# Kernel optimization log

Measured on AMD Instinct MI355X. Metric: run time of the kernel, lower is better.

## Reference

```python
import jax, jax.numpy as jnp
import numpy as np

B = 262144
NUM_CLASSES = 100
D = 128            # embedding_latent_dim and MLP width
VQ_DIM = 64        # vq_embedding_dim
VQ_K = 512         # vq_num_embeddings
A = 64             # action_dim
SQUISH = 1.0
COMMIT = 0.25


def _dense_params(key, fan_in, fan_out, scale=None):
    # he_uniform-like init; exact init distribution irrelevant for correctness baseline
    kw, kb = jax.random.split(key)
    lim = np.sqrt(6.0 / fan_in)
    W = jax.random.uniform(kw, (fan_in, fan_out), minval=-lim, maxval=lim, dtype=jnp.float32)
    b = jnp.zeros((fan_out,), dtype=jnp.float32)
    return W, b


def setup_inputs() -> dict:
    key = jax.random.key(0)
    ks = jax.random.split(key, 16)
    obs = jax.random.randint(ks[0], (B,), 0, NUM_CLASSES)
    embed = jax.random.normal(ks[1], (NUM_CLASSES, D), dtype=jnp.float32)
    W0, b0 = _dense_params(ks[2], D, D)
    W1, b1 = _dense_params(ks[3], D, D)
    W2, b2 = _dense_params(ks[4], D, D)
    Wp, bp = _dense_params(ks[5], D, VQ_DIM)
    lim = np.sqrt(3.0 / VQ_DIM)  # variance_scaling fan_in uniform
    vq_emb = jax.random.uniform(ks[6], (VQ_K, VQ_DIM), minval=-lim, maxval=lim, dtype=jnp.float32)
    Wa = 0.01 * jax.random.normal(ks[7], (VQ_DIM, A), dtype=jnp.float32)
    ba = jnp.zeros((A,), dtype=jnp.float32)
    Ws = 0.01 * jax.random.normal(ks[8], (VQ_DIM, A), dtype=jnp.float32)
    bs = jnp.zeros((A,), dtype=jnp.float32)
    Wc0, bc0 = _dense_params(ks[9], VQ_DIM, 128)
    Wc1, bc1 = _dense_params(ks[10], 128, 128)
    Wc2, bc2 = _dense_params(ks[11], 128, 32)
    Wc3, bc3 = _dense_params(ks[12], 32, 1)
    return dict(obs=obs, embed=embed, W0=W0, b0=b0, W1=W1, b1=b1, W2=W2, b2=b2,
                Wp=Wp, bp=bp, vq_emb=vq_emb, Wa=Wa, ba=ba, Ws=Ws, bs=bs,
                Wc0=Wc0, bc0=bc0, Wc1=Wc1, bc1=bc1, Wc2=Wc2, bc2=bc2, Wc3=Wc3, bc3=bc3)


def reference(obs, embed, W0, b0, W1, b1, W2, b2, Wp, bp, vq_emb,
              Wa, ba, Ws, bs, Wc0, bc0, Wc1, bc1, Wc2, bc2, Wc3, bc3):
    # class embedding lookup: [B, D]
    y = embed[obs]
    z = jax.nn.relu(y @ W0 + b0)
    z = jax.nn.relu(z @ W1 + b1)
    z = jax.nn.relu(z @ W2 + b2)
    z = z @ Wp + bp  # project to vq_embedding_dim: [B, 64]
    # --- VectorQuantizer ---
    # pairwise squared distances [B, K] via expansion trick
    dists = (jnp.sum(z * z, axis=1, keepdims=True)
             - 2.0 * (z @ vq_emb.T)
             + jnp.sum(vq_emb * vq_emb, axis=1)[None, :])
    encoding_indices = jnp.argmin(dists, axis=1)  # [B]
    quantized = vq_emb[encoding_indices]          # gather == onehot @ emb
    q_ste = z + jax.lax.stop_gradient(quantized - z)  # straight-through
    e_latent = jnp.mean((jax.lax.stop_gradient(q_ste) - z) ** 2)
    q_latent = jnp.mean((q_ste - jax.lax.stop_gradient(z)) ** 2)
    vq_loss = q_latent + COMMIT * e_latent
    # actor heads
    actor_mean = jax.nn.sigmoid(q_ste @ Wa + ba)
    scale_diag = jax.nn.sigmoid(q_ste @ Ws + bs) * SQUISH + 1e-8
    # critic stack
    c = jax.nn.sigmoid(q_ste @ Wc0 + bc0)
    c = jax.nn.sigmoid(c @ Wc1 + bc1)
    c = jax.nn.sigmoid(c @ Wc2 + bc2)
    critic = jnp.squeeze(c @ Wc3 + bc3, axis=-1)
    return actor_mean, scale_diag, critic, vq_loss, encoding_indices
```

## Files before the change

kernel.cpp:

```cpp
#include <hip/hip_runtime.h>
#include <hip/hip_bf16.h>
#include <math.h>

#define NCLS 100
#define DD   128
#define VQD  64
#define VQK  512

__device__ __forceinline__ float sigmoidf_(float x) { return 1.0f / (1.0f + expf(-x)); }

__global__ __launch_bounds__(128) void class_forward(
    const float* __restrict__ embed,
    const float* __restrict__ W0, const float* __restrict__ b0,
    const float* __restrict__ W1, const float* __restrict__ b1,
    const float* __restrict__ W2, const float* __restrict__ b2,
    const float* __restrict__ Wp, const float* __restrict__ bp,
    const float* __restrict__ vq,
    const float* __restrict__ Wa, const float* __restrict__ ba,
    const float* __restrict__ Ws, const float* __restrict__ bs,
    const float* __restrict__ Wc0, const float* __restrict__ bc0,
    const float* __restrict__ Wc1, const float* __restrict__ bc1,
    const float* __restrict__ Wc2, const float* __restrict__ bc2,
    const float* __restrict__ Wc3, const float* __restrict__ bc3,
    float* __restrict__ am_c, float* __restrict__ sd_c,
    float* __restrict__ cr_c, float* __restrict__ ms_c, int* __restrict__ id_c,
    unsigned int* __restrict__ counts)
{
    __shared__ float ya[128], za[128], q64[64], qs[64], red[128];
    __shared__ int   redi[128];
    const int c = blockIdx.x;
    const int t = threadIdx.x;

    if (c == 0 && t < NCLS) counts[t] = 0u;

    ya[t] = embed[c * DD + t];
    __syncthreads();

    float acc = b0[t];
    #pragma unroll 16
    for (int k = 0; k < 128; ++k) acc = fmaf(ya[k], W0[k * 128 + t], acc);
    za[t] = fmaxf(acc, 0.0f);
    __syncthreads();

    acc = b1[t];
    #pragma unroll 16
    for (int k = 0; k < 128; ++k) acc = fmaf(za[k], W1[k * 128 + t], acc);
    ya[t] = fmaxf(acc, 0.0f);
    __syncthreads();

    acc = b2[t];
    #pragma unroll 16
    for (int k = 0; k < 128; ++k) acc = fmaf(ya[k], W2[k * 128 + t], acc);
    za[t] = fmaxf(acc, 0.0f);
    __syncthreads();

    if (t < 64) {
        float a2 = bp[t];
        #pragma unroll 16
        for (int k = 0; k < 128; ++k) a2 = fmaf(za[k], Wp[k * 64 + t], a2);
        q64[t] = a2;
    }
    __syncthreads();

    if (t < 64) { red[t] = q64[t] * q64[t]; } else red[t] = 0.0f;
    __syncthreads();
    for (int s = 64; s > 0; s >>= 1) { if (t < s) red[t] += red[t + s]; __syncthreads(); }
    const float zz = red[0];
    __syncthreads();

    float bestv = 3.4e38f;
    int   besti = 0;
    for (int cc = t; cc < VQK; cc += 128) {
        const float* e = vq + cc * VQD;
        float dot = 0.0f, esq = 0.0f;
        #pragma unroll 16
        for (int k = 0; k < VQD; ++k) {
            float ev = e[k];
            dot = fmaf(q64[k], ev, dot);
            esq = fmaf(ev, ev, esq);
        }
        float d = (zz - 2.0f * dot) + esq;
        if (d < bestv) { bestv = d; besti = cc; }
    }
    red[t] = bestv; redi[t] = besti;
    __syncthreads();
    for (int s = 64; s > 0; s >>= 1) {
        if (t < s) {
            float v = red[t + s]; int i2 = redi[t + s];
            if (v < red[t] || (v == red[t] && i2 < redi[t])) { red[t] = v; redi[t] = i2; }
        }
        __syncthreads();
    }
    const int best = redi[0];
    __syncthreads();

    if (t < 64) {
        float z  = q64[t];
        float qq = vq[best * VQD + t];
        float q_ste = z + (qq - z);
        qs[t] = q_ste;
        float dd = q_ste - z;
        red[t] = dd * dd;
    } else red[t] = 0.0f;
    __syncthreads();
    for (int s = 64; s > 0; s >>= 1) { if (t < s) red[t] += red[t + s]; __syncthreads(); }
    if (t == 0) { ms_c[c] = red[0]; id_c[c] = best; }

    {
        const int j = t & 63;
        const float* W = (t < 64) ? Wa : Ws;
        float a2 = (t < 64) ? ba[j] : bs[j];
        #pragma unroll 16
        for (int k = 0; k < 64; ++k) a2 = fmaf(qs[k], W[k * 64 + j], a2);
        float s = sigmoidf_(a2);
        if (t < 64) am_c[c * 64 + j] = s;
        else        sd_c[c * 64 + j] = s * 1.0f + 1e-8f;
    }

    acc = bc0[t];
    #pragma unroll 16
    for (int k = 0; k < 64; ++k) acc = fmaf(qs[k], Wc0[k * 128 + t], acc);
    ya[t] = sigmoidf_(acc);
    __syncthreads();

    acc = bc1[t];
    #pragma unroll 16
    for (int k = 0; k < 128; ++k) acc = fmaf(ya[k], Wc1[k * 128 + t], acc);
    za[t] = sigmoidf_(acc);
    __syncthreads();

    if (t < 32) {
        float a2 = bc2[t];
        #pragma unroll 16
        for (int k = 0; k < 128; ++k) a2 = fmaf(za[k], Wc2[k * 32 + t], a2);
        q64[t] = sigmoidf_(a2);
    }
    __syncthreads();

    if (t == 0) {
        float a2 = bc3[0];
        for (int k = 0; k < 32; ++k) a2 = fmaf(q64[k], Wc3[k], a2);
        cr_c[c] = a2;
    }
}

__global__ __launch_bounds__(256) void scatter_vec(
    const int* __restrict__ obs,
    const float4* __restrict__ amc, const float4* __restrict__ sdc,
    const float* __restrict__ crc,  const int* __restrict__ idc,
    float4* __restrict__ out_am, float4* __restrict__ out_sd,
    float* __restrict__ out_cr,  float* __restrict__ out_idx, int n4)
{
    const int e4 = blockIdx.x * 256 + threadIdx.x;
    if (e4 >= n4) return;
    const int i  = e4 >> 4;
    const int d4 = e4 & 15;
    const int c  = obs[i];
    const int off = (c << 4) + d4;
    out_am[e4] = amc[off];
    out_sd[e4] = sdc[off];
    if (d4 == 0) {
        out_cr[i]  = crc[c];
        out_idx[i] = (float)idc[c];
    }
}

__global__ __launch_bounds__(256) void hist_obs(
    const int* __restrict__ obs, unsigned int* __restrict__ counts, int n)
{
    __shared__ unsigned int h[NCLS];
    const int t = threadIdx.x;
    if (t < NCLS) h[t] = 0u;
    __syncthreads();
    for (int i = blockIdx.x * blockDim.x + t; i < n; i += gridDim.x * blockDim.x)
        atomicAdd(&h[obs[i]], 1u);
    __syncthreads();
    if (t < NCLS) atomicAdd(&counts[t], h[t]);
}

__global__ __launch_bounds__(128) void finalize_vq(
    const unsigned int* __restrict__ counts, const float* __restrict__ ms,
    float* __restrict__ out, int n)
{
    __shared__ double sd[128];
    const int t = threadIdx.x;
    double a = 0.0;
    if (t < NCLS) a = (double)counts[t] * (double)ms[t];
    sd[t] = a;
    __syncthreads();
    for (int s = 64; s > 0; s >>= 1) { if (t < s) sd[t] += sd[t + s]; __syncthreads(); }
    if (t == 0) out[0] = (float)(1.25 * sd[0] / ((double)n * 64.0));
}

extern "C" void kernel_launch(void* const* d_in, const int* in_sizes, int n_in,
                              void* d_out, int out_size, void* d_ws, size_t ws_size,
                              hipStream_t stream)
{
    const int*   obs   = (const int*)d_in[0];
    const float* embed = (const float*)d_in[1];
    const float* W0  = (const float*)d_in[2];   const float* b0  = (const float*)d_in[3];
    const float* W1  = (const float*)d_in[4];   const float* b1  = (const float*)d_in[5];
    const float* W2  = (const float*)d_in[6];   const float* b2  = (const float*)d_in[7];
    const float* Wp  = (const float*)d_in[8];   const float* bp  = (const float*)d_in[9];
    const float* vq  = (const float*)d_in[10];
    const float* Wa  = (const float*)d_in[11];  const float* ba  = (const float*)d_in[12];
    const float* Ws  = (const float*)d_in[13];  const float* bs  = (const float*)d_in[14];
    const float* Wc0 = (const float*)d_in[15];  const float* bc0 = (const float*)d_in[16];
    const float* Wc1 = (const float*)d_in[17];  const float* bc1 = (const float*)d_in[18];
    const float* Wc2 = (const float*)d_in[19];  const float* bc2 = (const float*)d_in[20];
    const float* Wc3 = (const float*)d_in[21];  const float* bc3 = (const float*)d_in[22];

    const int n = in_sizes[0];

    float* ws_f  = (float*)d_ws;
    float* am_c  = ws_f;
    float* sd_c  = am_c + NCLS * 64;
    float* cr_c  = sd_c + NCLS * 64;
    float* ms_c  = cr_c + NCLS;
    int*   id_c  = (int*)(ms_c + NCLS);
    unsigned int* counts = (unsigned int*)(id_c + NCLS);

    float* out     = (float*)d_out;
    float* out_am  = out;
    float* out_sd  = out + (size_t)n * 64;
    float* out_cr  = out + (size_t)n * 128;
    float* out_vq  = out_cr + n;
    float* out_idx = out_vq + 1;

    class_forward<<<NCLS, 128, 0, stream>>>(
        embed, W0, b0, W1, b1, W2, b2, Wp, bp, vq,
        Wa, ba, Ws, bs, Wc0, bc0, Wc1, bc1, Wc2, bc2, Wc3, bc3,
        am_c, sd_c, cr_c, ms_c, id_c, counts);

    const int n4 = n * 16;
    scatter_vec<<<(n4 + 255) / 256, 256, 0, stream>>>(
        obs, (const float4*)am_c, (const float4*)sd_c, cr_c, id_c,
        (float4*)out_am, (float4*)out_sd, out_cr, out_idx, n4);

    hist_obs<<<512, 256, 0, stream>>>(obs, counts, n);

    finalize_vq<<<1, 128, 0, stream>>>(counts, ms_c, out_vq, n);
}
```

Before: 250.0 us.

## Fuse observation histogram into class kernel and VQ-loss finalize into scatter

Computes per-block partial histograms of obs inside the class_forward kernel, writing them to a partial-count buffer with no global atomics. The block-0 tail of the scatter kernel then sums the partials and computes the VQ loss. This drops two kernel launches and the global counts zeroing. The trade-off is that the 100 class blocks each scan a slice of obs after their MLP work, and block 0 of the scatter kernel does extra serial reduction work.

```diff
diff --git a/kernel.cpp b/kernel.cpp
--- a/kernel.cpp
+++ b/kernel.cpp
@@ -6,6 +6,8 @@
 #define DD   128
 #define VQD  64
 #define VQK  512
+
+typedef float f32x4 __attribute__((ext_vector_type(4)));
 
 __device__ __forceinline__ float sigmoidf_(float x) { return 1.0f / (1.0f + expf(-x)); }
 
@@ -22,18 +24,19 @@
     const float* __restrict__ Wc1, const float* __restrict__ bc1,
     const float* __restrict__ Wc2, const float* __restrict__ bc2,
     const float* __restrict__ Wc3, const float* __restrict__ bc3,
+    const int* __restrict__ obs, int nn,
     float* __restrict__ am_c, float* __restrict__ sd_c,
     float* __restrict__ cr_c, float* __restrict__ ms_c, int* __restrict__ id_c,
-    unsigned int* __restrict__ counts)
+    unsigned int* __restrict__ hist_part)
 {
     __shared__ float ya[128], za[128], q64[64], qs[64], red[128];
     __shared__ int   redi[128];
+    __shared__ unsigned int h[NCLS];
     const int c = blockIdx.x;
     const int t = threadIdx.x;
 
-    if (c == 0 && t < NCLS) counts[t] = 0u;
-
     ya[t] = embed[c * DD + t];
+    if (t < NCLS) h[t] = 0u;
     __syncthreads();
 
     float acc = b0[t];
@@ -142,54 +145,51 @@
         for (int k = 0; k < 32; ++k) a2 = fmaf(q64[k], Wc3[k], a2);
         cr_c[c] = a2;
     }
+
+    const int chunk = (nn + NCLS - 1) / NCLS;
+    const int i0 = c * chunk;
+    int i1 = i0 + chunk; if (i1 > nn) i1 = nn;
+    for (int i = i0 + t; i < i1; i += 128) atomicAdd(&h[obs[i]], 1u);
+    __syncthreads();
+    if (t < NCLS) hist_part[c * NCLS + t] = h[t];
 }
 
-__global__ __launch_bounds__(256) void scatter_vec(
+__global__ __launch_bounds__(256) void scatter_all(
     const int* __restrict__ obs,
-    const float4* __restrict__ amc, const float4* __restrict__ sdc,
+    const f32x4* __restrict__ amc, const f32x4* __restrict__ sdc,
     const float* __restrict__ crc,  const int* __restrict__ idc,
-    float4* __restrict__ out_am, float4* __restrict__ out_sd,
-    float* __restrict__ out_cr,  float* __restrict__ out_idx, int n4)
+    const float* __restrict__ msc,  const unsigned int* __restrict__ hist_part,
+    f32x4* __restrict__ out_am, f32x4* __restrict__ out_sd,
+    float* __restrict__ out_cr,  float* __restrict__ out_idx,
+    float* __restrict__ out_vq, int n4, int n)
 {
-    const int e4 = blockIdx.x * 256 + threadIdx.x;
-    if (e4 >= n4) return;
-    const int i  = e4 >> 4;
-    const int d4 = e4 & 15;
-    const int c  = obs[i];
-    const int off = (c << 4) + d4;
-    out_am[e4] = amc[off];
-    out_sd[e4] = sdc[off];
-    if (d4 == 0) {
-        out_cr[i]  = crc[c];
-        out_idx[i] = (float)idc[c];
-    }
-}
-
-__global__ __launch_bounds__(256) void hist_obs(
-    const int* __restrict__ obs, unsigned int* __restrict__ counts, int n)
-{
-    __shared__ unsigned int h[NCLS];
-    const int t = threadIdx.x;
-    if (t < NCLS) h[t] = 0u;
-    __syncthreads();
-    for (int i = blockIdx.x * blockDim.x + t; i < n; i += gridDim.x * blockDim.x)
-        atomicAdd(&h[obs[i]], 1u);
-    __syncthreads();
-    if (t < NCLS) atomicAdd(&counts[t], h[t]);
-}
-
-__global__ __launch_bounds__(128) void finalize_vq(
-    const unsigned int* __restrict__ counts, const float* __restrict__ ms,
-    float* __restrict__ out, int n)
-{
-    __shared__ double sd[128];
-    const int t = threadIdx.x;
-    double a = 0.0;
-    if (t < NCLS) a = (double)counts[t] * (double)ms[t];
-    sd[t] = a;
-    __syncthreads();
-    for (int s = 64; s > 0; s >>= 1) { if (t < s) sd[t] += sd[t + s]; __syncthreads(); }
-    if (t == 0) out[0] = (float)(1.25 * sd[0] / ((double)n * 64.0));
+    const int t  = threadIdx.x;
+    const int e4 = blockIdx.x * 256 + t;
+    if (e4 < n4) {
+        const int i  = e4 >> 4;
+        const int d4 = e4 & 15;
+        const int c  = obs[i];
+        const int off = (c << 4) + d4;
+        out_am[e4] = amc[off];
+        out_sd[e4] = sdc[off];
+        if (d4 == 0) {
+            out_cr[i]  = crc[c];
+            out_idx[i] = (float)idc[c];
+        }
+    }
+    if (blockIdx.x == 0) {
+        __shared__ double sd_[128];
+        double a = 0.0;
+        if (t < NCLS) {
+            unsigned int cnt = 0u;
+            for (int b = 0; b < NCLS; ++b) cnt += hist_part[b * NCLS + t];
+            a = (double)cnt * (double)msc[t];
+        }
+        if (t < 128) sd_[t] = a;
+        __syncthreads();
+        for (int s = 64; s > 0; s >>= 1) { if (t < s) sd_[t] += sd_[t + s]; __syncthreads(); }
+        if (t == 0) out_vq[0] = (float)(1.25 * sd_[0] / ((double)n * 64.0));
+    }
 }
 
 extern "C" void kernel_launch(void* const* d_in, const int* in_sizes, int n_in,
@@ -218,7 +218,7 @@
     float* cr_c  = sd_c + NCLS * 64;
     float* ms_c  = cr_c + NCLS;
     int*   id_c  = (int*)(ms_c + NCLS);
-    unsigned int* counts = (unsigned int*)(id_c + NCLS);
+    unsigned int* hist_part = (unsigned int*)(id_c + NCLS);
 
     float* out     = (float*)d_out;
     float* out_am  = out;
@@ -230,14 +230,11 @@
     class_forward<<<NCLS, 128, 0, stream>>>(
         embed, W0, b0, W1, b1, W2, b2, Wp, bp, vq,
         Wa, ba, Ws, bs, Wc0, bc0, Wc1, bc1, Wc2, bc2, Wc3, bc3,
-        am_c, sd_c, cr_c, ms_c, id_c, counts);
+        obs, n,
+        am_c, sd_c, cr_c, ms_c, id_c, hist_part);
 
     const int n4 = n * 16;
-    scatter_vec<<<(n4 + 255) / 256, 256, 0, stream>>>(
-        obs, (const float4*)am_c, (const float4*)sd_c, cr_c, id_c,
-        (float4*)out_am, (float4*)out_sd, out_cr, out_idx, n4);
-
-    hist_obs<<<512, 256, 0, stream>>>(obs, counts, n);
-
-    finalize_vq<<<1, 128, 0, stream>>>(counts, ms_c, out_vq, n);
+    scatter_all<<<(n4 + 255) / 256, 256, 0, stream>>>(
+        obs, (const f32x4*)am_c, (const f32x4*)sd_c, cr_c, id_c, ms_c, hist_part,
+        (f32x4*)out_am, (f32x4*)out_sd, out_cr, out_idx, out_vq, n4, n);
 }
```

New measurement: 233.8 us. 6.5% less time.
